# Performance work log

Measured on AMD Instinct MI355X. Metric: run time of the kernel, lower is better.

The kernel has to match this reference:

```python
import jax, jax.numpy as jnp
import numpy as np

B, N, T, F, D, R, K, L, E = 4, 2000, 50, 10, 64, 8, 16, 3, 32


def setup_inputs() -> dict:
    key = jax.random.key(0)
    ks = jax.random.split(key, 12)
    rn = lambda k, shape, sc: (jax.random.normal(k, shape, jnp.float32) * sc)
    return {
        "X": jax.random.normal(ks[0], (B, N, T, F), jnp.float32),
        "neighbors": jax.random.randint(ks[1], (B, R, N, K), 0, N + 1),
        "gru_W": rn(ks[2], (F, 3 * D), 0.1),
        "gru_U": rn(ks[3], (D, 3 * D), 0.1),
        "gru_b": jnp.zeros((2, 3 * D), jnp.float32),
        "rel_emb": rn(ks[4], (R, E), 0.1),
        "proj_W": rn(ks[5], (R, D, D), 0.05),
        "proj_b": jnp.zeros((R, D), jnp.float32),
        "satt_W": rn(ks[6], (R, 2 * D + E), 0.05),
        "satt_b": jnp.zeros((R,), jnp.float32),
        "ratt_W": rn(ks[7], (2 * D + E,), 0.05),
        "ratt_b": jnp.zeros((), jnp.float32),
        "pred_W": rn(ks[8], (D, L), 0.05),
        "pred_b": jnp.zeros((L,), jnp.float32),
    }


def leaky(x):  # tf.nn.leaky_relu default alpha=0.2
    return jnp.where(x >= 0, x, 0.2 * x)


def gru(x, W, U, b):
    # Keras GRU (reset_after=True), gate order [z, r, h]. x: (M, T, F)
    xp = x @ W + b[0]                      # (M, T, 3D) input projections, precomputed
    h0 = jnp.zeros((x.shape[0], U.shape[0]), x.dtype)

    def step(h, xt):
        rec = h @ U + b[1]
        xz, xr, xh = jnp.split(xt, 3, axis=-1)
        rz, rr, rh = jnp.split(rec, 3, axis=-1)
        z = jax.nn.sigmoid(xz + rz)
        r = jax.nn.sigmoid(xr + rr)
        hh = jnp.tanh(xh + r * rh)
        return z * h + (1.0 - z) * hh, None

    h, _ = jax.lax.scan(step, h0, jnp.swapaxes(xp, 0, 1))
    return h


def reference(X, neighbors, gru_W, gru_U, gru_b, rel_emb, proj_W, proj_b,
              satt_W, satt_b, ratt_W, ratt_b, pred_W, pred_b):
    b, n, t, f = X.shape
    d = gru_U.shape[0]

    # --- GRU feature extraction (dropout inactive at inference) ---
    node = gru(X.reshape(b * n, t, f), gru_W, gru_U, gru_b).reshape(b, n, d)
    padded = jnp.concatenate([jnp.zeros((b, 1, d), node.dtype), node], axis=1)  # (B, N+1, D)

    # --- per-relation neighbor gather + projection ---
    neigh_raw = jax.vmap(lambda nf, idx: nf[idx])(padded, neighbors)            # (B, R, N, K, D)
    neigh = leaky(jnp.einsum('brnkd,rde->brnke', neigh_raw, proj_W)
                  + proj_b[None, :, None, None, :])                              # (B, R, N, K, D)

    cur = node                                                                   # (B, N, D)

    # --- state attention: Dense(1) on concat[cur, neigh, rel_emb], split weights ---
    w_cur, w_ngh, w_rel = satt_W[:, :d], satt_W[:, d:2 * d], satt_W[:, 2 * d:]
    s_cur = jnp.einsum('bnd,rd->brn', cur, w_cur)                                # (B, R, N)
    s_ngh = jnp.einsum('brnkd,rd->brnk', neigh, w_ngh)                           # (B, R, N, K)
    s_rel = jnp.einsum('re,re->r', rel_emb, w_rel) + satt_b                      # (R,)
    scores = leaky(s_cur[:, :, :, None] + s_ngh + s_rel[None, :, None, None])
    scores = scores + jnp.where(neighbors == 0, -1e9, 0.0).astype(scores.dtype)  # mask padding node
    att = jax.nn.softmax(scores, axis=-1)                                        # over K
    rel_rep = jnp.einsum('brnk,brnkd->brnd', att, neigh)                         # (B, R, N, D)

    # --- relation attention ---
    rep_t = jnp.transpose(rel_rep, (0, 2, 1, 3))                                 # (B, N, R, D)
    r_cur, r_rep, r_emb = ratt_W[:d], ratt_W[d:2 * d], ratt_W[2 * d:]
    rs = leaky(jnp.einsum('bnd,d->bn', cur, r_cur)[:, :, None]
               + jnp.einsum('bnrd,d->bnr', rep_t, r_rep)
               + (rel_emb @ r_emb)[None, None, :] + ratt_b)                      # (B, N, R)
    ratt = jax.nn.softmax(rs, axis=-1)
    agg = jnp.einsum('bnr,bnrd->bnd', ratt, rep_t)
    updated = cur + agg

    # --- prediction head ---
    return jax.nn.softmax(updated @ pred_W + pred_b)
```

## Files before the change

kernel.cpp:

```cpp
#include <hip/hip_runtime.h>
#include <hip/hip_bf16.h>
#include <cstddef>
#include <cstring>

constexpr int cB=4, cN=2000, cT=50, cF=10, cD=64, cR=8, cK=16, cE=32;
constexpr int NODES = cB*cN;
constexpr int N1    = cN+1;
constexpr int ROWS2 = cB*N1;

#define DEV static __device__ __forceinline__

typedef __attribute__((ext_vector_type(8))) short    bf16x8;
typedef __attribute__((ext_vector_type(8))) _Float16 f16x8;
typedef __attribute__((ext_vector_type(4))) float    f32x4;
typedef __attribute__((ext_vector_type(4))) int      i32x4;

DEV float leaky(float x){ return fmaxf(x, 0.2f*x); }
DEV float wsumall(float v){
  v += __shfl_xor(v,32,64); v += __shfl_xor(v,16,64); v += __shfl_xor(v,8,64);
  v += __shfl_xor(v,4,64);  v += __shfl_xor(v,2,64);  v += __shfl_xor(v,1,64);
  return v;
}
DEV unsigned fu(float f){ return __float_as_uint(f); }
DEV unsigned rne16(float f){
  unsigned u = fu(f);
  return (u + 0x7FFFu + ((u>>16)&1u)) >> 16;
}
DEV unsigned f16b(float f){
  _Float16 h = (_Float16)f;
  unsigned short u; __builtin_memcpy(&u, &h, 2);
  return (unsigned)u;
}
DEV f16x8 packh(unsigned a, unsigned b, unsigned c2, unsigned d){
  union { i32x4 i; f16x8 h; } u;
  u.i = (i32x4){(int)a,(int)b,(int)c2,(int)d};
  return u.h;
}
DEV f16x8 asf16(i32x4 v){
  union { i32x4 i; f16x8 h; } u; u.i = v; return u.h;
}
DEV f32x4 MF16(f16x8 a, f16x8 b, f32x4 c){
  return __builtin_amdgcn_mfma_f32_16x16x32_f16(a, b, c, 0, 0, 0);
}
DEV float bfu(unsigned short u){ return __uint_as_float(((unsigned)u)<<16); }
DEV float ex2(float x){ float r; asm("v_exp_f32 %0, %1" : "=v"(r) : "v"(x)); return r; }

__global__ __launch_bounds__(256, 2) void k_gru(const float* __restrict__ X,
    const float* __restrict__ gW, const float* __restrict__ gU,
    const float* __restrict__ gb, const float* __restrict__ pW,
    const float* __restrict__ pb, const float* __restrict__ sattW,
    float* __restrict__ node, unsigned short* __restrict__ actb,
    float* __restrict__ sng2)
{
  __shared__ unsigned sF[2][512];

  const int tid  = threadIdx.x;
  const int lane = tid & 63;
  const int w    = tid >> 6;
  const int c    = lane & 15;
  const int kg   = lane >> 4;
  const int nb   = (int)blockIdx.x * 16;
  const int col  = 16*w + c;
  const int bb   = nb / cN;

  const float SZ = -1.4426950408889634f;
  const float SH =  2.8853900817779268f;

  f16x8 Uf[2][3];
  #pragma unroll
  for (int s=0;s<2;++s){
    #pragma unroll
    for (int cls=0; cls<3; ++cls){
      const float sc = (cls==2) ? SH : SZ;
      const int n = cls*64 + col;
      unsigned wd[4];
      #pragma unroll
      for (int p=0;p<4;++p){
        int d0 = s*32 + kg*8 + 2*p;
        wd[p] = f16b(sc*gU[d0*192 + n]) | (f16b(sc*gU[(d0+1)*192 + n]) << 16);
      }
      Uf[s][cls] = packh(wd[0],wd[1],wd[2],wd[3]);
    }
  }
  const float bzt = SZ*(gb[col] + gb[192+col]);
  const float brt = SZ*(gb[64+col] + gb[256+col]);
  const float bh0 = SH* gb[128+col];
  const float bh1 = SH* gb[320+col];
  f16x8 BXf[3];
  #pragma unroll
  for (int cls=0; cls<3; ++cls){
    const float sc = (cls==2) ? SH : SZ;
    const float bv = (cls==0) ? bzt : (cls==1 ? brt : bh0);
    const int n = cls*64 + col;
    unsigned wd[4];
    #pragma unroll
    for (int p=0;p<4;++p){
      int f = kg*4 + p;
      unsigned v = (f < cF) ? f16b(sc*gW[f*192 + n]) : ((f == cF) ? f16b(bv) : 0u);
      wd[p] = v;
    }
    BXf[cls] = packh(wd[0],wd[1],wd[2],wd[3]);
  }

  for (int i2 = tid; i2 < 512; i2 += 256) sF[0][i2] = 0u;
  f32x4 ho = {0.f,0.f,0.f,0.f};
  __syncthreads();

  float xc[4], xn[4];
  const float* Xb = X + (size_t)(nb + c)*cT*cF;
  #pragma unroll
  for (int p=0;p<4;++p){
    int f = 4*kg+p;
    float fill = (f == cF) ? 1.0f : 0.0f;
    xc[p] = (f < cF) ? Xb[0*cF + f] : fill;
    xn[p] = (f < cF) ? Xb[1*cF + f] : fill;
  }

  const unsigned sw2   = (unsigned)((c&7)<<2);
  const unsigned base0 = ((unsigned)(c*32 + kg*4))      ^ sw2;
  const unsigned base1 = ((unsigned)(c*32 + 16 + kg*4)) ^ sw2;
  unsigned hws[4];
  #pragma unroll
  for (int reg=0; reg<4; ++reg){
    int nodei = kg*4 + reg;
    hws[reg] = (((unsigned)(nodei*32 + (col>>1))) ^ ((unsigned)((nodei&7)<<2)))*2
               + (unsigned)(col&1);
  }
  const f32x4 zq = {0.f,0.f,0.f,0.f};

  for (int t = 0; t < cT; ++t){
    f16x8 xf = packh(f16b(xc[0]), f16b(xc[1]), f16b(xc[2]), f16b(xc[3]));
    #pragma unroll
    for (int p=0;p<4;++p) xc[p] = xn[p];
    {
      int tn = (t+2 < cT) ? t+2 : cT-1;
      #pragma unroll
      for (int p=0;p<4;++p){
        int f = 4*kg+p;
        float fill = (f == cF) ? 1.0f : 0.0f;
        xn[p] = (f < cF) ? Xb[(size_t)tn*cF + f] : fill;
      }
    }

    const unsigned* sr = sF[t & 1];
    i32x4 q0 = *(const i32x4*)(sr + base0);
    i32x4 q1 = *(const i32x4*)(sr + base1);
    f16x8 ha = asf16(q0), hb = asf16(q1);

    f32x4 aZ  = MF16(xf, BXf[0], zq);
    f32x4 aR  = MF16(xf, BXf[1], zq);
    f32x4 aXh = MF16(xf, BXf[2], zq);
    f32x4 aHc = {bh1,bh1,bh1,bh1};
    aZ  = MF16(ha, Uf[0][0], aZ);  aZ  = MF16(hb, Uf[1][0], aZ);
    aR  = MF16(ha, Uf[0][1], aR);  aR  = MF16(hb, Uf[1][1], aR);
    aHc = MF16(ha, Uf[0][2], aHc); aHc = MF16(hb, Uf[1][2], aHc);

    unsigned short* swr = (unsigned short*)sF[(t & 1) ^ 1];
    #pragma unroll
    for (int reg=0; reg<4; ++reg){
      float z   = __builtin_amdgcn_rcpf(1.0f + ex2(aZ[reg]));
      float r   = __builtin_amdgcn_rcpf(1.0f + ex2(aR[reg]));
      float phv = __builtin_fmaf(r, aHc[reg], aXh[reg]);
      float th  = __builtin_fmaf(-2.0f, __builtin_amdgcn_rcpf(ex2(phv) + 1.0f), 1.0f);
      float hn  = __builtin_fmaf(z, ho[reg]-th, th);
      ho[reg] = hn;
      swr[hws[reg]] = (unsigned short)f16b(hn);
    }
    asm volatile("s_waitcnt lgkmcnt(0)" ::: "memory");
    __builtin_amdgcn_s_barrier();
  }

  #pragma unroll
  for (int reg=0; reg<4; ++reg)
    node[(size_t)(nb + kg*4 + reg)*cD + col] = ho[reg];

  {
    const unsigned* sr = &sF[0][0];
    i32x4 q0 = *(const i32x4*)(sr + base0);
    i32x4 q1 = *(const i32x4*)(sr + base1);
    f16x8 ha = asf16(q0), hb = asf16(q1);

    const int qbase = nb + bb + 1;
    #pragma unroll
    for (int rr=0; rr<2; ++rr){
      const int r = 2*w + rr;
      const float* Pr = pW + (size_t)r*cD*cD;
      f16x8 PB[4][2];
      float pbv[4], wnv[4];
      #pragma unroll
      for (int cb=0; cb<4; ++cb){
        const int e = 16*cb + c;
        #pragma unroll
        for (int s2=0;s2<2;++s2){
          unsigned wd[4];
          #pragma unroll
          for (int p=0;p<4;++p){
            int d0 = s2*32 + kg*8 + 2*p;
            wd[p] = f16b(Pr[(size_t)d0*cD + e]) | (f16b(Pr[(size_t)(d0+1)*cD + e]) << 16);
          }
          PB[cb][s2] = packh(wd[0],wd[1],wd[2],wd[3]);
        }
        pbv[cb] = pb[r*cD + e];
        wnv[cb] = sattW[r*(2*cD+cE) + cD + e];
      }
      float sp[4] = {0.f,0.f,0.f,0.f};
      #pragma unroll
      for (int cb=0; cb<4; ++cb){
        f32x4 acc = {pbv[cb],pbv[cb],pbv[cb],pbv[cb]};
        acc = MF16(ha, PB[cb][0], acc);
        acc = MF16(hb, PB[cb][1], acc);
        #pragma unroll
        for (int reg=0; reg<4; ++reg){
          float o = leaky(acc[reg]);
          int qrow = qbase + kg*4 + reg;
          actb[((size_t)r*ROWS2 + qrow)*cD + 16*cb + c] = (unsigned short)rne16(o);
          sp[reg] = __builtin_fmaf(o, wnv[cb], sp[reg]);
        }
      }
      #pragma unroll
      for (int reg=0; reg<4; ++reg){
        float s2 = sp[reg];
        s2 += __shfl_xor(s2,1,64); s2 += __shfl_xor(s2,2,64);
        s2 += __shfl_xor(s2,4,64); s2 += __shfl_xor(s2,8,64);
        if (c == 0) sng2[(size_t)r*ROWS2 + qbase + kg*4 + reg] = s2;
      }
    }
  }

  if ((blockIdx.x % (cN/16)) == 0){
    #pragma unroll
    for (int rr=0; rr<2; ++rr){
      const int r = 2*w + rr;
      float v0 = leaky(pb[r*cD + lane]);
      float wv = sattW[r*(2*cD+cE) + cD + lane];
      actb[((size_t)r*ROWS2 + (size_t)bb*N1)*cD + lane] = (unsigned short)rne16(v0);
      float s2 = wsumall(v0 * wv);
      if (lane == 0) sng2[(size_t)r*ROWS2 + (size_t)bb*N1] = s2;
    }
  }
}

__global__ __launch_bounds__(256) void k_attn(const float* __restrict__ node,
    const int* __restrict__ nbrs, const float* __restrict__ sattW,
    const float* __restrict__ sattb, const float* __restrict__ rattW,
    const float* __restrict__ rattb, const float* __restrict__ predW,
    const float* __restrict__ predb, const float* __restrict__ relemb,
    const unsigned short* __restrict__ actb, const float* __restrict__ sng2,
    float* __restrict__ out)
{
  __shared__ float sSA[cR][cD];
  __shared__ float sSrel[cR], sRremb[cR];
  __shared__ float sAtt[4][cR][cK];
  __shared__ int   sOff[4][cR][cK];
  const int tid = threadIdx.x;
  for (int i=tid; i<cR*cD; i+=256) sSA[i>>6][i&63] = sattW[(i>>6)*(2*cD+cE) + (i&63)];
  if (tid < 64){
    int r = tid >> 3, j0 = (tid & 7)*4;
    float a = 0.f, b2 = 0.f;
    #pragma unroll
    for (int j=0;j<4;++j){
      float re = relemb[r*cE + j0 + j];
      a  += re * sattW[r*(2*cD+cE) + 2*cD + j0 + j];
      b2 += re * rattW[2*cD + j0 + j];
    }
    a  += __shfl_xor(a,1,64);  a  += __shfl_xor(a,2,64);  a  += __shfl_xor(a,4,64);
    b2 += __shfl_xor(b2,1,64); b2 += __shfl_xor(b2,2,64); b2 += __shfl_xor(b2,4,64);
    if ((tid & 7) == 0){ sSrel[r] = a + sattb[r]; sRremb[r] = b2; }
  }
  __syncthreads();

  const int wave = tid >> 6, lane = tid & 63;
  const int gn = (int)blockIdx.x*4 + wave;
  const int b = __builtin_amdgcn_readfirstlane(gn / cN);
  const int n = __builtin_amdgcn_readfirstlane(gn % cN);

  const float cur = node[(size_t)gn*cD + lane];

  float scr[8];
  #pragma unroll
  for (int r=0; r<8; ++r) scr[r] = wsumall(cur * sSA[r][lane]);

  const int g = lane >> 4, k = lane & 15;
  #pragma unroll
  for (int half=0; half<2; ++half){
    int r = half*4 + g;
    float sc0 = half==0 ? (g==0?scr[0]:g==1?scr[1]:g==2?scr[2]:scr[3])
                        : (g==0?scr[4]:g==1?scr[5]:g==2?scr[6]:scr[7]);
    int idx = nbrs[(((size_t)b*cR + r)*cN + n)*cK + k];
    int o = r*ROWS2 + b*N1 + idx;
    float sv = sng2[o];
    float sc = leaky(sc0 + sv + sSrel[r]);
    if (idx == 0) sc -= 1e9f;
    float mx = sc;
    mx = fmaxf(mx, __shfl_xor(mx,1,64)); mx = fmaxf(mx, __shfl_xor(mx,2,64));
    mx = fmaxf(mx, __shfl_xor(mx,4,64)); mx = fmaxf(mx, __shfl_xor(mx,8,64));
    float ex = __expf(sc - mx);
    float sm = ex;
    sm += __shfl_xor(sm,1,64); sm += __shfl_xor(sm,2,64);
    sm += __shfl_xor(sm,4,64); sm += __shfl_xor(sm,8,64);
    sAtt[wave][r][k] = ex/sm;
    sOff[wave][r][k] = o;
  }
  __syncthreads();

  float facc[8];
  #pragma unroll
  for (int r=0; r<8; ++r){
    float a0=0.f, a1=0.f;
    #pragma unroll
    for (int kk=0; kk<cK; kk+=2){
      float w0 = sAtt[wave][r][kk],   w1 = sAtt[wave][r][kk+1];
      int   o0 = sOff[wave][r][kk],   o1 = sOff[wave][r][kk+1];
      a0 += w0 * bfu(actb[(size_t)o0*cD + lane]);
      a1 += w1 * bfu(actb[(size_t)o1*cD + lane]);
    }
    facc[r] = a0 + a1;
  }

  const float rcur = rattW[lane], rrep = rattW[cD + lane];
  const float rb   = rattb[0];
  const float c0 = wsumall(cur * rcur);
  float rs[8];
  #pragma unroll
  for (int r=0; r<8; ++r) rs[r] = leaky(c0 + wsumall(facc[r]*rrep) + sRremb[r] + rb);
  float mx = rs[0];
  #pragma unroll
  for (int r=1; r<8; ++r) mx = fmaxf(mx, rs[r]);
  float es = 0.f; float ratt[8];
  #pragma unroll
  for (int r=0; r<8; ++r){ ratt[r] = __expf(rs[r]-mx); es += ratt[r]; }
  float inv = 1.f/es;
  float agg = 0.f;
  #pragma unroll
  for (int r=0; r<8; ++r) agg += (ratt[r]*inv) * facc[r];
  const float upd = cur + agg;

  float l0 = wsumall(upd * predW[lane*3 + 0]);
  float l1 = wsumall(upd * predW[lane*3 + 1]);
  float l2 = wsumall(upd * predW[lane*3 + 2]);
  if (lane == 0){
    l0 += predb[0]; l1 += predb[1]; l2 += predb[2];
    float m2 = fmaxf(l0, fmaxf(l1, l2));
    float e0 = __expf(l0-m2), e1 = __expf(l1-m2), e2 = __expf(l2-m2);
    float is = 1.f/(e0+e1+e2);
    out[(size_t)gn*3+0] = e0*is;
    out[(size_t)gn*3+1] = e1*is;
    out[(size_t)gn*3+2] = e2*is;
  }
}

extern "C" void kernel_launch(void* const* d_in, const int* in_sizes, int n_in,
                              void* d_out, int out_size, void* d_ws, size_t ws_size,
                              hipStream_t stream)
{
  const float* X      = (const float*)d_in[0];
  const int*   nbrs   = (const int*)  d_in[1];
  const float* gW     = (const float*)d_in[2];
  const float* gU     = (const float*)d_in[3];
  const float* gb     = (const float*)d_in[4];
  const float* relemb = (const float*)d_in[5];
  const float* pW     = (const float*)d_in[6];
  const float* pb     = (const float*)d_in[7];
  const float* sattW  = (const float*)d_in[8];
  const float* sattb  = (const float*)d_in[9];
  const float* rattW  = (const float*)d_in[10];
  const float* rattb  = (const float*)d_in[11];
  const float* predW  = (const float*)d_in[12];
  const float* predb  = (const float*)d_in[13];
  float* out = (float*)d_out;

  float*          node  = (float*)d_ws;
  unsigned short* actb  = (unsigned short*)(node + (size_t)NODES*cD);
  float*          sng2  = (float*)(actb + (size_t)cR*ROWS2*cD);

  k_gru <<<NODES/16, 256, 0, stream>>>(X, gW, gU, gb, pW, pb, sattW,
                                       node, actb, sng2);
  k_attn<<<NODES/4, 256, 0, stream>>>(node, nbrs, sattW, sattb, rattW, rattb,
                                      predW, predb, relemb, actb, sng2, out);
}
```

Measured before the change: 81.03 us.

## Split GRU hidden state into hi/lo fp16 and halve nodes per block

The GRU recurrent state is now stored as a pair of fp16 values (high part plus residual) and the recurrent MFMA is run on both, which recovers near-fp32 accuracy for h@U. Each block now handles 8 nodes instead of 16, so twice as many blocks are launched and the occupancy hint rises to 4. Half of each 16-row MFMA tile is zero padding, which wastes matrix work, and the recurrent MFMA count doubles. The apparent aim is more parallelism across CUs to hide the latency of the serial time loop, at the cost of extra compute and LDS traffic.

```diff
diff --git a/kernel.cpp b/kernel.cpp
--- a/kernel.cpp
+++ b/kernel.cpp
@@ -7,6 +7,7 @@
 constexpr int NODES = cB*cN;
 constexpr int N1    = cN+1;
 constexpr int ROWS2 = cB*N1;
+constexpr int TN    = 8;
 
 #define DEV static __device__ __forceinline__
 
@@ -31,6 +32,14 @@
   unsigned short u; __builtin_memcpy(&u, &h, 2);
   return (unsigned)u;
 }
+DEV void split16(float f, unsigned &hi, unsigned &lo){
+  _Float16 h = (_Float16)f;
+  float r = f - (float)h;
+  _Float16 l = (_Float16)r;
+  unsigned short uh, ul;
+  __builtin_memcpy(&uh, &h, 2); __builtin_memcpy(&ul, &l, 2);
+  hi = uh; lo = ul;
+}
 DEV f16x8 packh(unsigned a, unsigned b, unsigned c2, unsigned d){
   union { i32x4 i; f16x8 h; } u;
   u.i = (i32x4){(int)a,(int)b,(int)c2,(int)d};
@@ -45,23 +54,26 @@
 DEV float bfu(unsigned short u){ return __uint_as_float(((unsigned)u)<<16); }
 DEV float ex2(float x){ float r; asm("v_exp_f32 %0, %1" : "=v"(r) : "v"(x)); return r; }
 
-__global__ __launch_bounds__(256, 2) void k_gru(const float* __restrict__ X,
+__global__ __launch_bounds__(256, 4) void k_gru(const float* __restrict__ X,
     const float* __restrict__ gW, const float* __restrict__ gU,
     const float* __restrict__ gb, const float* __restrict__ pW,
     const float* __restrict__ pb, const float* __restrict__ sattW,
     float* __restrict__ node, unsigned short* __restrict__ actb,
     float* __restrict__ sng2)
 {
-  __shared__ unsigned sF[2][512];
+  __shared__ unsigned sHh[2][512];
+  __shared__ unsigned sHl[2][512];
 
   const int tid  = threadIdx.x;
   const int lane = tid & 63;
   const int w    = tid >> 6;
   const int c    = lane & 15;
   const int kg   = lane >> 4;
-  const int nb   = (int)blockIdx.x * 16;
+  const int nb   = (int)blockIdx.x * TN;
   const int col  = 16*w + c;
   const int bb   = nb / cN;
+  const bool rowok = (c < TN);
+  const bool outok = (kg < 2);
 
   const float SZ = -1.4426950408889634f;
   const float SH =  2.8853900817779268f;
@@ -102,7 +114,7 @@
     BXf[cls] = packh(wd[0],wd[1],wd[2],wd[3]);
   }
 
-  for (int i2 = tid; i2 < 512; i2 += 256) sF[0][i2] = 0u;
+  for (int i2 = tid; i2 < 512; i2 += 256){ sHh[0][i2] = 0u; sHl[0][i2] = 0u; }
   f32x4 ho = {0.f,0.f,0.f,0.f};
   __syncthreads();
 
@@ -111,9 +123,9 @@
   #pragma unroll
   for (int p=0;p<4;++p){
     int f = 4*kg+p;
-    float fill = (f == cF) ? 1.0f : 0.0f;
-    xc[p] = (f < cF) ? Xb[0*cF + f] : fill;
-    xn[p] = (f < cF) ? Xb[1*cF + f] : fill;
+    float fill = (rowok && f == cF) ? 1.0f : 0.0f;
+    xc[p] = (rowok && f < cF) ? Xb[0*cF + f] : fill;
+    xn[p] = (rowok && f < cF) ? Xb[1*cF + f] : fill;
   }
 
   const unsigned sw2   = (unsigned)((c&7)<<2);
@@ -137,25 +149,33 @@
       #pragma unroll
       for (int p=0;p<4;++p){
         int f = 4*kg+p;
-        float fill = (f == cF) ? 1.0f : 0.0f;
-        xn[p] = (f < cF) ? Xb[(size_t)tn*cF + f] : fill;
+        float fill = (rowok && f == cF) ? 1.0f : 0.0f;
+        xn[p] = (rowok && f < cF) ? Xb[(size_t)tn*cF + f] : fill;
       }
     }
 
-    const unsigned* sr = sF[t & 1];
-    i32x4 q0 = *(const i32x4*)(sr + base0);
-    i32x4 q1 = *(const i32x4*)(sr + base1);
-    f16x8 ha = asf16(q0), hb = asf16(q1);
+    const unsigned* srh = sHh[t & 1];
+    const unsigned* srl = sHl[t & 1];
+    i32x4 qh0 = *(const i32x4*)(srh + base0);
+    i32x4 qh1 = *(const i32x4*)(srh + base1);
+    i32x4 ql0 = *(const i32x4*)(srl + base0);
+    i32x4 ql1 = *(const i32x4*)(srl + base1);
+    f16x8 hah = asf16(qh0), hbh = asf16(qh1);
+    f16x8 hal = asf16(ql0), hbl = asf16(ql1);
 
     f32x4 aZ  = MF16(xf, BXf[0], zq);
     f32x4 aR  = MF16(xf, BXf[1], zq);
     f32x4 aXh = MF16(xf, BXf[2], zq);
     f32x4 aHc = {bh1,bh1,bh1,bh1};
-    aZ  = MF16(ha, Uf[0][0], aZ);  aZ  = MF16(hb, Uf[1][0], aZ);
-    aR  = MF16(ha, Uf[0][1], aR);  aR  = MF16(hb, Uf[1][1], aR);
-    aHc = MF16(ha, Uf[0][2], aHc); aHc = MF16(hb, Uf[1][2], aHc);
-
-    unsigned short* swr = (unsigned short*)sF[(t & 1) ^ 1];
+    aZ  = MF16(hah, Uf[0][0], aZ);  aZ  = MF16(hbh, Uf[1][0], aZ);
+    aR  = MF16(hah, Uf[0][1], aR);  aR  = MF16(hbh, Uf[1][1], aR);
+    aHc = MF16(hah, Uf[0][2], aHc); aHc = MF16(hbh, Uf[1][2], aHc);
+    aZ  = MF16(hal, Uf[0][0], aZ);  aZ  = MF16(hbl, Uf[1][0], aZ);
+    aR  = MF16(hal, Uf[0][1], aR);  aR  = MF16(hbl, Uf[1][1], aR);
+    aHc = MF16(hal, Uf[0][2], aHc); aHc = MF16(hbl, Uf[1][2], aHc);
+
+    unsigned short* swh = (unsigned short*)sHh[(t & 1) ^ 1];
+    unsigned short* swl = (unsigned short*)sHl[(t & 1) ^ 1];
     #pragma unroll
     for (int reg=0; reg<4; ++reg){
       float z   = __builtin_amdgcn_rcpf(1.0f + ex2(aZ[reg]));
@@ -164,20 +184,24 @@
       float th  = __builtin_fmaf(-2.0f, __builtin_amdgcn_rcpf(ex2(phv) + 1.0f), 1.0f);
       float hn  = __builtin_fmaf(z, ho[reg]-th, th);
       ho[reg] = hn;
-      swr[hws[reg]] = (unsigned short)f16b(hn);
+      unsigned hi, lo; split16(hn, hi, lo);
+      swh[hws[reg]] = (unsigned short)hi;
+      swl[hws[reg]] = (unsigned short)lo;
     }
     asm volatile("s_waitcnt lgkmcnt(0)" ::: "memory");
     __builtin_amdgcn_s_barrier();
   }
 
-  #pragma unroll
-  for (int reg=0; reg<4; ++reg)
-    node[(size_t)(nb + kg*4 + reg)*cD + col] = ho[reg];
+  if (outok){
+    #pragma unroll
+    for (int reg=0; reg<4; ++reg)
+      node[(size_t)(nb + kg*4 + reg)*cD + col] = ho[reg];
+  }
 
   {
-    const unsigned* sr = &sF[0][0];
-    i32x4 q0 = *(const i32x4*)(sr + base0);
-    i32x4 q1 = *(const i32x4*)(sr + base1);
+    const unsigned* srh = &sHh[0][0];
+    i32x4 q0 = *(const i32x4*)(srh + base0);
+    i32x4 q1 = *(const i32x4*)(srh + base1);
     f16x8 ha = asf16(q0), hb = asf16(q1);
 
     const int qbase = nb + bb + 1;
@@ -212,8 +236,10 @@
         #pragma unroll
         for (int reg=0; reg<4; ++reg){
           float o = leaky(acc[reg]);
-          int qrow = qbase + kg*4 + reg;
-          actb[((size_t)r*ROWS2 + qrow)*cD + 16*cb + c] = (unsigned short)rne16(o);
+          if (outok){
+            int qrow = qbase + kg*4 + reg;
+            actb[((size_t)r*ROWS2 + qrow)*cD + 16*cb + c] = (unsigned short)rne16(o);
+          }
           sp[reg] = __builtin_fmaf(o, wnv[cb], sp[reg]);
         }
       }
@@ -222,12 +248,12 @@
         float s2 = sp[reg];
         s2 += __shfl_xor(s2,1,64); s2 += __shfl_xor(s2,2,64);
         s2 += __shfl_xor(s2,4,64); s2 += __shfl_xor(s2,8,64);
-        if (c == 0) sng2[(size_t)r*ROWS2 + qbase + kg*4 + reg] = s2;
+        if (c == 0 && outok) sng2[(size_t)r*ROWS2 + qbase + kg*4 + reg] = s2;
       }
     }
   }
 
-  if ((blockIdx.x % (cN/16)) == 0){
+  if ((nb % cN) == 0){
     #pragma unroll
     for (int rr=0; rr<2; ++rr){
       const int r = 2*w + rr;
@@ -373,7 +399,7 @@
   unsigned short* actb  = (unsigned short*)(node + (size_t)NODES*cD);
   float*          sng2  = (float*)(actb + (size_t)cR*ROWS2*cD);
 
-  k_gru <<<NODES/16, 256, 0, stream>>>(X, gW, gU, gb, pW, pb, sattW,
+  k_gru <<<NODES/TN, 256, 0, stream>>>(X, gW, gU, gb, pW, pb, sattW,
                                        node, actb, sng2);
   k_attn<<<NODES/4, 256, 0, stream>>>(node, nbrs, sattW, sattb, rattW, rattb,
                                       predW, predb, relemb, actb, sng2, out);
```

New measurement: 109.5 us, median of 3. +35.1%, slower.
